# Kernel tuning notes

Hardware: AMD Instinct MI355X
Metric: run time of the kernel (lower is better)

The kernel has to match this reference:

```python
import jax, jax.numpy as jnp
import numpy as np

N_NODES = 50000
N_EDGES = 500000
N_GRAPHS = 64
IN_DIM = 64
HID = 128
N_LAYERS = 2
BN_EPS = 1e-5


def setup_inputs() -> dict:
    key = jax.random.key(0)
    ks = jax.random.split(key, 12)
    x = jax.random.normal(ks[0], (N_NODES, IN_DIM), dtype=jnp.float32)
    edge_index = jax.random.randint(ks[1], (2, N_EDGES), 0, N_NODES, dtype=jnp.int64)
    batch = jnp.sort(jax.random.randint(ks[2], (N_NODES,), 0, N_GRAPHS, dtype=jnp.int64))
    s = 0.05
    W_enc = jax.random.normal(ks[3], (IN_DIM, HID), dtype=jnp.float32) * s
    b_enc = jnp.zeros((HID,), dtype=jnp.float32)
    Wc = jax.random.normal(ks[4], (N_LAYERS, HID, HID), dtype=jnp.float32) * s
    bc = jnp.zeros((N_LAYERS, HID), dtype=jnp.float32)
    gamma = jnp.ones((N_LAYERS, HID), dtype=jnp.float32)
    beta = jnp.zeros((N_LAYERS, HID), dtype=jnp.float32)
    MID = HID // 2
    W1 = jax.random.normal(ks[5], (HID, MID), dtype=jnp.float32) * s
    b1 = jnp.zeros((MID,), dtype=jnp.float32)
    W2 = jax.random.normal(ks[6], (MID, 1), dtype=jnp.float32) * s
    b2 = jnp.zeros((1,), dtype=jnp.float32)
    return {"x": x, "edge_index": edge_index, "batch": batch,
            "W_enc": W_enc, "b_enc": b_enc, "Wc": Wc, "bc": bc,
            "gamma": gamma, "beta": beta, "W1": W1, "b1": b1,
            "W2": W2, "b2": b2}


def _gcn_conv(h, src, dst, norm, W, b, n_nodes):
    # h: [N, HID]; src/dst: [E+N] (self-loops included); norm: [E+N]
    h = h @ W                                   # [N, HID]
    msg = h[src] * norm[:, None]                # gather + normalize
    out = jax.ops.segment_sum(msg, dst, num_segments=n_nodes)  # scatter-add
    return out + b


def _batch_norm(h, g, b):
    mu = jnp.mean(h, axis=0)
    var = jnp.var(h, axis=0)
    return (h - mu) * jax.lax.rsqrt(var + BN_EPS) * g + b


def reference(x, edge_index, batch, W_enc, b_enc, Wc, bc, gamma, beta, W1, b1, W2, b2):
    n = x.shape[0]
    loop = jnp.arange(n, dtype=edge_index.dtype)
    src = jnp.concatenate([edge_index[0], loop])   # [E+N]
    dst = jnp.concatenate([edge_index[1], loop])
    # symmetric GCN normalization with self-loops: deg over target index
    deg = jax.ops.segment_sum(jnp.ones_like(dst, dtype=x.dtype), dst, num_segments=n)
    dinv = jax.lax.rsqrt(deg)                      # deg >= 1 due to self-loops
    norm = dinv[src] * dinv[dst]                   # [E+N]

    h = x @ W_enc + b_enc                          # node encoder
    for l in range(Wc.shape[0]):
        h = _gcn_conv(h, src, dst, norm, Wc[l], bc[l], n)
        h = _batch_norm(h, gamma[l], beta[l])
        h = jax.nn.relu(h)                         # dropout inactive (eval)

    # global mean pool over graphs
    pooled = jax.ops.segment_sum(h, batch, num_segments=N_GRAPHS)
    counts = jax.ops.segment_sum(jnp.ones((n,), dtype=h.dtype), batch, num_segments=N_GRAPHS)
    pooled = pooled / jnp.maximum(counts, 1.0)[:, None]

    z = jax.nn.relu(pooled @ W1 + b1)
    out = jax.nn.sigmoid(z @ W2 + b2)              # [B, 1]
    return out.squeeze(-1)                          # [B]
```

## Files before the change

kernel.cpp:

```cpp
#include <hip/hip_runtime.h>
#include <hip/hip_bf16.h>
#include <hip/hip_fp16.h>
#include <math.h>


typedef _Float16 f16x8 __attribute__((ext_vector_type(8)));
typedef float f32x4 __attribute__((ext_vector_type(4)));

__device__ inline unsigned pack2(float a, float b) {
  union { __half2 h; unsigned u; } p;
  p.h = __floats2half2_rn(a, b);
  return p.u;
}
__device__ inline float2 unpack2(unsigned u) {
  union { unsigned u; __half2 h; } p;
  p.u = u;
  return __half22float2(p.h);
}

__global__ __launch_bounds__(256) void k_init(int* __restrict__ deg,
                                              float* __restrict__ pooled,
                                              float* __restrict__ bnstat,
                                              int N) {
  int i = blockIdx.x * 256 + threadIdx.x;
  if (i < N) deg[i] = 1;
  if (i < 64 * 128) pooled[i] = 0.f;
  if (i < 4096) bnstat[i] = 0.f;
}

__global__ __launch_bounds__(256) void k_deg(const int* __restrict__ ei, int E,
                                             int* __restrict__ deg) {
  int i = blockIdx.x * 256 + threadIdx.x;
  if (i < E) atomicAdd(&deg[ei[E + i]], 1);
}

__global__ __launch_bounds__(256) void k_scan_a(const int* __restrict__ deg, int N,
                                                int* __restrict__ rowptr,
                                                int* __restrict__ blksum) {
  __shared__ int s[256];
  int t = threadIdx.x;
  int i = blockIdx.x * 256 + t;
  int v = (i < N) ? deg[i] : 0;
  s[t] = v;
  __syncthreads();
  for (int off = 1; off < 256; off <<= 1) {
    int x = (t >= off) ? s[t - off] : 0;
    __syncthreads();
    s[t] += x;
    __syncthreads();
  }
  if (i < N) rowptr[i] = s[t] - v;
  if (t == 255) blksum[blockIdx.x] = s[255];
}

__global__ __launch_bounds__(256) void k_scan_b(int* __restrict__ blksum, int nb) {
  __shared__ int s[256];
  int t = threadIdx.x;
  int v = (t < nb) ? blksum[t] : 0;
  s[t] = v;
  __syncthreads();
  for (int off = 1; off < 256; off <<= 1) {
    int x = (t >= off) ? s[t - off] : 0;
    __syncthreads();
    s[t] += x;
    __syncthreads();
  }
  if (t < nb) blksum[t] = s[t] - v;
}

__global__ __launch_bounds__(256) void k_scan_c(const int* __restrict__ deg, int N,
                                                int total,
                                                const int* __restrict__ blksum,
                                                int* __restrict__ rowptr,
                                                int* __restrict__ cursor,
                                                float* __restrict__ dinv) {
  int i = blockIdx.x * 256 + threadIdx.x;
  if (i < N) {
    int rp = rowptr[i] + blksum[blockIdx.x];
    rowptr[i] = rp;
    cursor[i] = rp;
    dinv[i] = rsqrtf((float)deg[i]);
  } else if (i == N) {
    rowptr[N] = total;
  }
}

__global__ __launch_bounds__(256) void k_fill(const int* __restrict__ ei, int E, int N,
                                              int* __restrict__ cursor,
                                              int* __restrict__ colx) {
  int i = blockIdx.x * 256 + threadIdx.x;
  if (i < E) {
    int s = ei[i];
    int d = ei[E + i];
    int pos = atomicAdd(&cursor[d], 1);
    colx[pos] = s;
  } else if (i < E + N) {
    int j = i - E;
    int pos = atomicAdd(&cursor[j], 1);
    colx[pos] = j;
  }
}

__global__ __launch_bounds__(128) void k_fold(const float* __restrict__ W_enc,
                                              const float* __restrict__ b_enc,
                                              const float* __restrict__ Wc0,
                                              unsigned short* __restrict__ MT,
                                              float* __restrict__ bfold) {
  int n = threadIdx.x;
  int k = blockIdx.x;
  const float* arow = (k < 64) ? (W_enc + (size_t)k * 128) : b_enc;
  float acc = 0.f;
  for (int j = 0; j < 128; j++) acc = fmaf(arow[j], Wc0[(size_t)j * 128 + n], acc);
  if (k < 64) ((__half*)MT)[(size_t)n * 64 + k] = __float2half(acc);
  else bfold[n] = acc;
}

__global__ __launch_bounds__(256) void k_wprep(const float* __restrict__ Wsrc,
                                               unsigned short* __restrict__ WT) {
  int i = blockIdx.x * 256 + threadIdx.x;
  int n = i & 127, k = i >> 7;
  ((__half*)WT)[(size_t)n * 128 + k] = __float2half(Wsrc[i]);
}

__global__ __launch_bounds__(256) void k_prep0(const float* __restrict__ x,
                                               const float* __restrict__ dinv,
                                               unsigned* __restrict__ xs2,
                                               int total ) {
  int i = blockIdx.x * 256 + threadIdx.x;
  if (i < total) {
    int row = i >> 4;
    float4 v = ((const float4*)x)[i];
    float d = dinv[row];
    uint2 o;
    o.x = pack2(v.x * d, v.y * d);
    o.y = pack2(v.z * d, v.w * d);
    ((uint2*)xs2)[i] = o;
  }
}

__global__ __launch_bounds__(256) void k_prep1(const unsigned short* __restrict__ H16,
                                               const float* __restrict__ scsh,
                                               const float* __restrict__ dinv,
                                               unsigned* __restrict__ hs2,
                                               int total ) {
  int i = blockIdx.x * 256 + threadIdx.x;
  if (i < total) {
    int row = i >> 5;
    int c4 = i & 31;
    uint2 hv = ((const uint2*)H16)[i];
    float2 h01 = unpack2(hv.x), h23 = unpack2(hv.y);
    float4 sc = ((const float4*)scsh)[c4];
    float4 sh = ((const float4*)(scsh + 128))[c4];
    float d = dinv[row];
    float a = fmaxf(fmaf(h01.x, sc.x, sh.x), 0.f) * d;
    float b = fmaxf(fmaf(h01.y, sc.y, sh.y), 0.f) * d;
    float c = fmaxf(fmaf(h23.x, sc.z, sh.z), 0.f) * d;
    float e = fmaxf(fmaf(h23.y, sc.w, sh.w), 0.f) * d;
    uint2 o;
    o.x = pack2(a, b);
    o.y = pack2(c, e);
    ((uint2*)hs2)[i] = o;
  }
}

__global__ __launch_bounds__(256) void k_agg0(const unsigned* __restrict__ xs,
                                              const int* __restrict__ rowptr,
                                              const int* __restrict__ colx,
                                              const float* __restrict__ dinv,
                                              unsigned* __restrict__ axh,
                                              float* __restrict__ w, int N) {
  int lane = threadIdx.x & 63;
  int wv = threadIdx.x >> 6;
  int half = lane >> 5;
  int l32 = lane & 31;
  int wid = blockIdx.x * 4 + wv;
  int nw = gridDim.x * 4;

  for (int base = 2 * wid; base < N; base += 2 * nw) {
    int i = base + half;
    if (i < N) {
      int beg = rowptr[i];
      int end = rowptr[i + 1];
      float sx = 0.f, sy = 0.f, sd = 0.f;
      int e = beg;
#pragma unroll 1
      for (; e + 4 <= end; e += 4) {
        int i0 = colx[e + 0], i1 = colx[e + 1], i2 = colx[e + 2], i3 = colx[e + 3];
        unsigned v0 = xs[(size_t)i0 * 32 + l32];
        unsigned v1 = xs[(size_t)i1 * 32 + l32];
        unsigned v2 = xs[(size_t)i2 * 32 + l32];
        unsigned v3 = xs[(size_t)i3 * 32 + l32];
        float d0 = dinv[i0], d1 = dinv[i1], d2 = dinv[i2], d3 = dinv[i3];
        float2 f0 = unpack2(v0), f1 = unpack2(v1), f2 = unpack2(v2), f3 = unpack2(v3);
        sx += (f0.x + f1.x) + (f2.x + f3.x);
        sy += (f0.y + f1.y) + (f2.y + f3.y);
        sd += (d0 + d1) + (d2 + d3);
      }
#pragma unroll 1
      for (; e < end; e++) {
        int sr = colx[e];
        float2 f = unpack2(xs[(size_t)sr * 32 + l32]);
        sx += f.x;
        sy += f.y;
        sd += dinv[sr];
      }
      float di = dinv[i];
      axh[(size_t)i * 32 + l32] = pack2(sx * di, sy * di);
      if (l32 == 0) w[i] = di * sd;
    }
  }
}

__global__ __launch_bounds__(256) void k_agg1(const uint2* __restrict__ hs,
                                              const int* __restrict__ rowptr,
                                              const int* __restrict__ colx,
                                              const float* __restrict__ dinv,
                                              uint2* __restrict__ a1h, int N) {
  int lane = threadIdx.x & 63;
  int wv = threadIdx.x >> 6;
  int half = lane >> 5;
  int l32 = lane & 31;
  int wid = blockIdx.x * 4 + wv;
  int nw = gridDim.x * 4;

  for (int base = 2 * wid; base < N; base += 2 * nw) {
    int i = base + half;
    if (i < N) {
      int beg = rowptr[i];
      int end = rowptr[i + 1];
      float4 s = make_float4(0.f, 0.f, 0.f, 0.f);
      int e = beg;
#pragma unroll 1
      for (; e + 4 <= end; e += 4) {
        int i0 = colx[e + 0], i1 = colx[e + 1], i2 = colx[e + 2], i3 = colx[e + 3];
        uint2 v0 = hs[(size_t)i0 * 32 + l32];
        uint2 v1 = hs[(size_t)i1 * 32 + l32];
        uint2 v2 = hs[(size_t)i2 * 32 + l32];
        uint2 v3 = hs[(size_t)i3 * 32 + l32];
        float2 a0 = unpack2(v0.x), b0 = unpack2(v0.y);
        float2 a1f = unpack2(v1.x), b1f = unpack2(v1.y);
        float2 a2 = unpack2(v2.x), b2 = unpack2(v2.y);
        float2 a3 = unpack2(v3.x), b3 = unpack2(v3.y);
        s.x += (a0.x + a1f.x) + (a2.x + a3.x);
        s.y += (a0.y + a1f.y) + (a2.y + a3.y);
        s.z += (b0.x + b1f.x) + (b2.x + b3.x);
        s.w += (b0.y + b1f.y) + (b2.y + b3.y);
      }
#pragma unroll 1
      for (; e < end; e++) {
        int sr = colx[e];
        uint2 v = hs[(size_t)sr * 32 + l32];
        float2 a = unpack2(v.x), b = unpack2(v.y);
        s.x += a.x; s.y += a.y; s.z += b.x; s.w += b.y;
      }
      float di = dinv[i];
      a1h[(size_t)i * 32 + l32] =
          make_uint2(pack2(s.x * di, s.y * di), pack2(s.z * di, s.w * di));
    }
  }
}

template <int K>
__global__ __launch_bounds__(256, 2) void k_gemm_f16(
    const unsigned short* __restrict__ Xh,
    const unsigned short* __restrict__ WT,
    const float* __restrict__ bias,
    const float* __restrict__ wvec,
    const float* __restrict__ bias2,
    float* __restrict__ stat,
    unsigned short* __restrict__ Yh,
    int N) {
  constexpr int KP = K + 8;
  constexpr int K8 = K / 8;
  __shared__ unsigned short Wl[128 * KP];
  __shared__ float red[4][2][128];

  for (int i = threadIdx.x; i < 128 * K8; i += 256) {
    int r = i / K8, c = i - r * K8;
    *(uint4*)&Wl[r * KP + c * 8] = ((const uint4*)(WT + (size_t)r * K))[c];
  }
  __syncthreads();

  int lane = threadIdx.x & 63;
  int wv = threadIdx.x >> 6;
  int l15 = lane & 15;
  int kg = lane >> 4;
  int tileRow = blockIdx.x * 64 + wv * 16;

  int arow = tileRow + l15;
  if (arow >= N) arow = N - 1;
  const unsigned short* xp = Xh + (size_t)arow * K + kg * 8;
  f16x8 af[K / 32];
#pragma unroll
  for (int j = 0; j < K / 32; j++) af[j] = *(const f16x8*)(xp + j * 32);

  f32x4 acc[8];
#pragma unroll
  for (int t = 0; t < 8; t++) acc[t] = {0.f, 0.f, 0.f, 0.f};

  const unsigned short* wb = &Wl[l15 * KP + kg * 8];
#pragma unroll
  for (int j = 0; j < K / 32; j++) {
#pragma unroll
    for (int t = 0; t < 8; t++) {
      f16x8 bf = *(const f16x8*)(wb + t * 16 * KP + j * 32);
      acc[t] = __builtin_amdgcn_mfma_f32_16x16x32_f16(af[j], bf, acc[t], 0, 0, 0);
    }
  }

  int rbase = tileRow + kg * 4;
  float wrow[4];
#pragma unroll
  for (int r = 0; r < 4; r++)
    wrow[r] = (wvec && rbase + r < N) ? wvec[rbase + r] : 0.f;

#pragma unroll
  for (int t = 0; t < 8; t++) {
    int ch = t * 16 + l15;
    float bb = bias[ch];
    float b2v = bias2 ? bias2[ch] : 0.f;
    float s = 0.f, q = 0.f;
#pragma unroll
    for (int r = 0; r < 4; r++) {
      int row = rbase + r;
      if (row < N) {
        float o = acc[t][r] + bb;
        if (wvec) o = fmaf(wrow[r], b2v, o);
        __half oh = __float2half(o);
        Yh[(size_t)row * 128 + ch] = *(unsigned short*)&oh;
        s += o;
        q += o * o;
      }
    }
    s += __shfl_xor(s, 16); s += __shfl_xor(s, 32);
    q += __shfl_xor(q, 16); q += __shfl_xor(q, 32);
    if (kg == 0) { red[wv][0][ch] = s; red[wv][1][ch] = q; }
  }
  __syncthreads();
  int st = threadIdx.x >> 7, ch2 = threadIdx.x & 127;
  float v = red[0][st][ch2] + red[1][st][ch2] + red[2][st][ch2] + red[3][st][ch2];
  atomicAdd(&stat[(blockIdx.x & 7) * 256 + st * 128 + ch2], v);
}

__global__ __launch_bounds__(128) void k_bnfinal(const float* __restrict__ stat,
                                                 const float* __restrict__ gamma,
                                                 const float* __restrict__ beta,
                                                 float invN,
                                                 float* __restrict__ scsh) {
  int c = threadIdx.x;
  float ssum = 0.f, qsum = 0.f;
#pragma unroll
  for (int rep = 0; rep < 8; rep++) {
    ssum += stat[rep * 256 + c];
    qsum += stat[rep * 256 + 128 + c];
  }
  float mu = ssum * invN;
  float var = qsum * invN - mu * mu;
  float sc = rsqrtf(var + 1e-5f) * gamma[c];
  scsh[c] = sc;
  scsh[128 + c] = beta[c] - mu * sc;
}

__global__ __launch_bounds__(128) void k_gstart(const int* __restrict__ batch, int N,
                                                int* __restrict__ gstart) {
  int g = threadIdx.x;
  if (g <= 64) {
    int lo = 0, hi = N;
    while (lo < hi) {
      int mid = (lo + hi) >> 1;
      if (batch[mid] < g) lo = mid + 1;
      else hi = mid;
    }
    gstart[g] = lo;
  }
}

__global__ __launch_bounds__(128) void k_pool(const unsigned short* __restrict__ H16,
                                              const float* __restrict__ scsh,
                                              const int* __restrict__ gstart,
                                              float* __restrict__ pooled) {
  int g = blockIdx.x >> 3;
  int part = blockIdx.x & 7;
  int c = threadIdx.x;
  float sc = scsh[c], sh = scsh[128 + c];
  int beg = gstart[g], end = gstart[g + 1];
  int len = end - beg;
  int pbeg = beg + (len * part) / 8;
  int pend = beg + (len * (part + 1)) / 8;
  float s = 0.f;
  for (int r = pbeg; r < pend; r++) {
    float v = __half2float(((const __half*)H16)[(size_t)r * 128 + c]);
    s += fmaxf(fmaf(v, sc, sh), 0.f);
  }
  atomicAdd(&pooled[g * 128 + c], s);
}

__global__ __launch_bounds__(256) void k_mlp(const float* __restrict__ pooled,
                                             const int* __restrict__ gstart,
                                             const float* __restrict__ W1,
                                             const float* __restrict__ b1,
                                             const float* __restrict__ W2,
                                             const float* __restrict__ b2,
                                             float* __restrict__ out) {
  __shared__ float P[64 * 128];
  __shared__ float Z[64 * 64];
  for (int i = threadIdx.x; i < 64 * 128; i += 256) {
    int g = i >> 7;
    int cnt = gstart[g + 1] - gstart[g];
    P[i] = pooled[i] / (float)(cnt > 1 ? cnt : 1);
  }
  __syncthreads();
  for (int i = threadIdx.x; i < 64 * 64; i += 256) {
    int g = i >> 6, m = i & 63;
    float acc = b1[m];
    for (int k = 0; k < 128; k++) acc += P[(g << 7) + k] * W1[k * 64 + m];
    Z[i] = fmaxf(acc, 0.f);
  }
  __syncthreads();
  if (threadIdx.x < 64) {
    int g = threadIdx.x;
    float acc = b2[0];
    for (int m = 0; m < 64; m++) acc += Z[(g << 6) + m] * W2[m];
    out[g] = 1.f / (1.f + expf(-acc));
  }
}


extern "C" void kernel_launch(void* const* d_in, const int* in_sizes, int n_in,
                              void* d_out, int out_size, void* d_ws, size_t ws_size,
                              hipStream_t stream) {
  const float* x      = (const float*)d_in[0];
  const int*   ei     = (const int*)d_in[1];
  const int*   batch  = (const int*)d_in[2];
  const float* W_enc  = (const float*)d_in[3];
  const float* b_enc  = (const float*)d_in[4];
  const float* Wc     = (const float*)d_in[5];
  const float* bc     = (const float*)d_in[6];
  const float* gamma  = (const float*)d_in[7];
  const float* beta   = (const float*)d_in[8];
  const float* W1     = (const float*)d_in[9];
  const float* b1     = (const float*)d_in[10];
  const float* W2     = (const float*)d_in[11];
  const float* b2     = (const float*)d_in[12];
  float* out = (float*)d_out;

  const int N = in_sizes[2];
  const int E = in_sizes[1] / 2;
  const int NL = in_sizes[6] / 128;

  size_t off = 0;
  auto alloc = [&](size_t bytes) {
    void* p = (char*)d_ws + off;
    off += (bytes + 255) & ~(size_t)255;
    return p;
  };
  unsigned short* h16 = (unsigned short*)alloc((size_t)N * 128 * 2);
  int*   deg    = (int*)alloc((size_t)N * 4);
  float* dinv   = (float*)alloc((size_t)N * 4);
  int*   rowptr = (int*)alloc((size_t)(N + 1) * 4);
  int*   cursor = (int*)alloc((size_t)N * 4);
  int*   colx   = (int*)alloc((size_t)(E + N) * 4);
  int*   blksum = (int*)alloc(1024 * 4);
  float* bnstat = (float*)alloc(4096 * 4);
  float* scsh   = (float*)alloc(512 * 4);
  float* pooled = (float*)alloc(64 * 128 * 4);
  int*   gstart = (int*)alloc(65 * 4);
  unsigned short* MT  = (unsigned short*)alloc(128 * 64 * 2);
  unsigned short* WT1 = (unsigned short*)alloc(128 * 128 * 2);
  float* bfold  = (float*)alloc(128 * 4);
  unsigned* xs  = (unsigned*)alloc((size_t)N * 64 * 2);
  unsigned* hs  = (unsigned*)alloc((size_t)N * 128 * 2);
  unsigned* axh = (unsigned*)alloc((size_t)N * 64 * 2);
  uint2*    a1h = (uint2*)alloc((size_t)N * 128 * 2);
  float* wv     = (float*)alloc((size_t)N * 4);

  int nbN = (N + 255) / 256;

  k_init<<<nbN, 256, 0, stream>>>(deg, pooled, bnstat, N);
  k_deg<<<(E + 255) / 256, 256, 0, stream>>>(ei, E, deg);
  k_scan_a<<<nbN, 256, 0, stream>>>(deg, N, rowptr, blksum);
  k_scan_b<<<1, 256, 0, stream>>>(blksum, nbN);
  k_scan_c<<<(N + 1 + 255) / 256, 256, 0, stream>>>(deg, N, E + N, blksum,
                                                    rowptr, cursor, dinv);
  k_fill<<<(E + N + 255) / 256, 256, 0, stream>>>(ei, E, N, cursor, colx);
  k_fold<<<65, 128, 0, stream>>>(W_enc, b_enc, Wc, MT, bfold);

  int tiles = (N + 63) / 64;

  k_prep0<<<(N * 16 + 255) / 256, 256, 0, stream>>>(x, dinv, xs, N * 16);
  k_agg0<<<2048, 256, 0, stream>>>(xs, rowptr, colx, dinv, axh, wv, N);
  k_gemm_f16<64><<<tiles, 256, 0, stream>>>(
      (const unsigned short*)axh, MT, bc, wv, bfold, bnstat, h16, N);
  k_bnfinal<<<1, 128, 0, stream>>>(bnstat, gamma, beta, 1.f / (float)N, scsh);

  for (int l = 1; l < NL; l++) {
    k_wprep<<<64, 256, 0, stream>>>(Wc + (size_t)l * 128 * 128, WT1);
    k_prep1<<<(N * 32 + 255) / 256, 256, 0, stream>>>(
        h16, scsh + (l - 1) * 256, dinv, hs, N * 32);
    k_agg1<<<2048, 256, 0, stream>>>((const uint2*)hs, rowptr, colx, dinv,
                                     a1h, N);
    k_gemm_f16<128><<<tiles, 256, 0, stream>>>(
        (const unsigned short*)a1h, WT1, bc + l * 128, nullptr, nullptr,
        bnstat + l * 2048, h16, N);
    k_bnfinal<<<1, 128, 0, stream>>>(bnstat + l * 2048, gamma + l * 128,
                                     beta + l * 128, 1.f / (float)N,
                                     scsh + l * 256);
  }

  k_gstart<<<1, 128, 0, stream>>>(batch, N, gstart);
  k_pool<<<64 * 8, 128, 0, stream>>>(h16, scsh + (NL - 1) * 256, gstart, pooled);
  k_mlp<<<1, 256, 0, stream>>>(pooled, gstart, W1, b1, W2, b2, out);
}
```

Before: 295.1 us.

## Merge setup kernels, fold BN finalize into consumers, widen agg0 gathers

Combines init, weight folding, layer-1 weight prep and graph-start search into one setup launch, and merges CSR fill with input prescaling. Removes the separate BN finalize and gstart kernels by recomputing scale/shift inside prep1 and pool blocks. Changes agg0 to 16 lanes per node with 8-byte loads, handling four nodes per wave. Fewer launches reduce per-kernel overhead, but every block now redundantly recomputes the BN statistics.

```diff
diff --git a/kernel.cpp b/kernel.cpp
--- a/kernel.cpp
+++ b/kernel.cpp
@@ -18,14 +18,55 @@
   return __half22float2(p.h);
 }
 
-__global__ __launch_bounds__(256) void k_init(int* __restrict__ deg,
-                                              float* __restrict__ pooled,
-                                              float* __restrict__ bnstat,
-                                              int N) {
-  int i = blockIdx.x * 256 + threadIdx.x;
-  if (i < N) deg[i] = 1;
-  if (i < 64 * 128) pooled[i] = 0.f;
-  if (i < 4096) bnstat[i] = 0.f;
+__global__ __launch_bounds__(256) void k_setup(
+    int* __restrict__ deg, float* __restrict__ pooled,
+    float* __restrict__ bnstat, int statTotal, int N, int nbN,
+    const float* __restrict__ W_enc, const float* __restrict__ b_enc,
+    const float* __restrict__ Wc, unsigned short* __restrict__ MT,
+    float* __restrict__ bfold, int NL,
+    const float* __restrict__ Wc1, unsigned short* __restrict__ WT1,
+    const int* __restrict__ batch, int* __restrict__ gstart) {
+  int b = blockIdx.x;
+  if (b < nbN) {
+    int i = b * 256 + threadIdx.x;
+    if (i < N) deg[i] = 1;
+    if (i < 64 * 128) pooled[i] = 0.f;
+    if (i < statTotal) bnstat[i] = 0.f;
+    return;
+  }
+  b -= nbN;
+  if (b < 65) {
+    if (threadIdx.x < 128) {
+      int n = threadIdx.x;
+      int k = b;
+      const float* arow = (k < 64) ? (W_enc + (size_t)k * 128) : b_enc;
+      float acc = 0.f;
+      for (int j = 0; j < 128; j++)
+        acc = fmaf(arow[j], Wc[(size_t)j * 128 + n], acc);
+      if (k < 64) ((__half*)MT)[(size_t)n * 64 + k] = __float2half(acc);
+      else bfold[n] = acc;
+    }
+    return;
+  }
+  b -= 65;
+  if (b < 64) {
+    if (NL > 1) {
+      int i = b * 256 + threadIdx.x;
+      int n = i & 127, k = i >> 7;
+      ((__half*)WT1)[(size_t)n * 128 + k] = __float2half(Wc1[i]);
+    }
+    return;
+  }
+  int g = threadIdx.x;
+  if (g <= 64) {
+    int lo = 0, hi = N;
+    while (lo < hi) {
+      int mid = (lo + hi) >> 1;
+      if (batch[mid] < g) lo = mid + 1;
+      else hi = mid;
+    }
+    gstart[g] = lo;
+  }
 }
 
 __global__ __launch_bounds__(256) void k_deg(const int* __restrict__ ei, int E,
@@ -85,49 +126,29 @@
   }
 }
 
-__global__ __launch_bounds__(256) void k_fill(const int* __restrict__ ei, int E, int N,
-                                              int* __restrict__ cursor,
-                                              int* __restrict__ colx) {
-  int i = blockIdx.x * 256 + threadIdx.x;
-  if (i < E) {
-    int s = ei[i];
-    int d = ei[E + i];
-    int pos = atomicAdd(&cursor[d], 1);
-    colx[pos] = s;
-  } else if (i < E + N) {
-    int j = i - E;
-    int pos = atomicAdd(&cursor[j], 1);
-    colx[pos] = j;
-  }
-}
-
-__global__ __launch_bounds__(128) void k_fold(const float* __restrict__ W_enc,
-                                              const float* __restrict__ b_enc,
-                                              const float* __restrict__ Wc0,
-                                              unsigned short* __restrict__ MT,
-                                              float* __restrict__ bfold) {
-  int n = threadIdx.x;
-  int k = blockIdx.x;
-  const float* arow = (k < 64) ? (W_enc + (size_t)k * 128) : b_enc;
-  float acc = 0.f;
-  for (int j = 0; j < 128; j++) acc = fmaf(arow[j], Wc0[(size_t)j * 128 + n], acc);
-  if (k < 64) ((__half*)MT)[(size_t)n * 64 + k] = __float2half(acc);
-  else bfold[n] = acc;
-}
-
-__global__ __launch_bounds__(256) void k_wprep(const float* __restrict__ Wsrc,
-                                               unsigned short* __restrict__ WT) {
-  int i = blockIdx.x * 256 + threadIdx.x;
-  int n = i & 127, k = i >> 7;
-  ((__half*)WT)[(size_t)n * 128 + k] = __float2half(Wsrc[i]);
-}
-
-__global__ __launch_bounds__(256) void k_prep0(const float* __restrict__ x,
-                                               const float* __restrict__ dinv,
-                                               unsigned* __restrict__ xs2,
-                                               int total ) {
-  int i = blockIdx.x * 256 + threadIdx.x;
-  if (i < total) {
+__global__ __launch_bounds__(256) void k_fillprep(
+    const int* __restrict__ ei, int E, int N, int nbEN,
+    int* __restrict__ cursor, int* __restrict__ colx,
+    const float* __restrict__ x, const float* __restrict__ dinv,
+    unsigned* __restrict__ xs2) {
+  int b = blockIdx.x;
+  if (b < nbEN) {
+    int i = b * 256 + threadIdx.x;
+    if (i < E) {
+      int s = ei[i];
+      int d = ei[E + i];
+      int pos = atomicAdd(&cursor[d], 1);
+      colx[pos] = s;
+    } else if (i < E + N) {
+      int j = i - E;
+      int pos = atomicAdd(&cursor[j], 1);
+      colx[pos] = j;
+    }
+    return;
+  }
+  b -= nbEN;
+  int i = b * 256 + threadIdx.x;
+  if (i < N * 16) {
     int row = i >> 4;
     float4 v = ((const float4*)x)[i];
     float d = dinv[row];
@@ -139,18 +160,37 @@
 }
 
 __global__ __launch_bounds__(256) void k_prep1(const unsigned short* __restrict__ H16,
-                                               const float* __restrict__ scsh,
+                                               const float* __restrict__ stat,
+                                               const float* __restrict__ gamma,
+                                               const float* __restrict__ beta,
+                                               float invN,
                                                const float* __restrict__ dinv,
                                                unsigned* __restrict__ hs2,
                                                int total ) {
+  __shared__ float scsh[256];
+  if (threadIdx.x < 128) {
+    int c = threadIdx.x;
+    float ss = 0.f, qs = 0.f;
+#pragma unroll
+    for (int r = 0; r < 8; r++) {
+      ss += stat[r * 256 + c];
+      qs += stat[r * 256 + 128 + c];
+    }
+    float mu = ss * invN;
+    float var = qs * invN - mu * mu;
+    float sc = rsqrtf(var + 1e-5f) * gamma[c];
+    scsh[c] = sc;
+    scsh[128 + c] = beta[c] - mu * sc;
+  }
+  __syncthreads();
   int i = blockIdx.x * 256 + threadIdx.x;
   if (i < total) {
     int row = i >> 5;
     int c4 = i & 31;
     uint2 hv = ((const uint2*)H16)[i];
     float2 h01 = unpack2(hv.x), h23 = unpack2(hv.y);
-    float4 sc = ((const float4*)scsh)[c4];
-    float4 sh = ((const float4*)(scsh + 128))[c4];
+    float4 sc = *(const float4*)&scsh[c4 * 4];
+    float4 sh = *(const float4*)&scsh[128 + c4 * 4];
     float d = dinv[row];
     float a = fmaxf(fmaf(h01.x, sc.x, sh.x), 0.f) * d;
     float b = fmaxf(fmaf(h01.y, sc.y, sh.y), 0.f) * d;
@@ -163,50 +203,56 @@
   }
 }
 
-__global__ __launch_bounds__(256) void k_agg0(const unsigned* __restrict__ xs,
+__global__ __launch_bounds__(256) void k_agg0(const uint2* __restrict__ xs,
                                               const int* __restrict__ rowptr,
                                               const int* __restrict__ colx,
                                               const float* __restrict__ dinv,
-                                              unsigned* __restrict__ axh,
+                                              uint2* __restrict__ axh,
                                               float* __restrict__ w, int N) {
   int lane = threadIdx.x & 63;
   int wv = threadIdx.x >> 6;
-  int half = lane >> 5;
-  int l32 = lane & 31;
+  int grp = lane >> 4;
+  int l16 = lane & 15;
   int wid = blockIdx.x * 4 + wv;
   int nw = gridDim.x * 4;
 
-  for (int base = 2 * wid; base < N; base += 2 * nw) {
-    int i = base + half;
+  for (int base = 4 * wid; base < N; base += 4 * nw) {
+    int i = base + grp;
     if (i < N) {
       int beg = rowptr[i];
       int end = rowptr[i + 1];
-      float sx = 0.f, sy = 0.f, sd = 0.f;
+      float s0 = 0.f, s1 = 0.f, s2 = 0.f, s3 = 0.f, sd = 0.f;
       int e = beg;
 #pragma unroll 1
       for (; e + 4 <= end; e += 4) {
         int i0 = colx[e + 0], i1 = colx[e + 1], i2 = colx[e + 2], i3 = colx[e + 3];
-        unsigned v0 = xs[(size_t)i0 * 32 + l32];
-        unsigned v1 = xs[(size_t)i1 * 32 + l32];
-        unsigned v2 = xs[(size_t)i2 * 32 + l32];
-        unsigned v3 = xs[(size_t)i3 * 32 + l32];
+        uint2 v0 = xs[(size_t)i0 * 16 + l16];
+        uint2 v1 = xs[(size_t)i1 * 16 + l16];
+        uint2 v2 = xs[(size_t)i2 * 16 + l16];
+        uint2 v3 = xs[(size_t)i3 * 16 + l16];
         float d0 = dinv[i0], d1 = dinv[i1], d2 = dinv[i2], d3 = dinv[i3];
-        float2 f0 = unpack2(v0), f1 = unpack2(v1), f2 = unpack2(v2), f3 = unpack2(v3);
-        sx += (f0.x + f1.x) + (f2.x + f3.x);
-        sy += (f0.y + f1.y) + (f2.y + f3.y);
+        float2 a0 = unpack2(v0.x), b0 = unpack2(v0.y);
+        float2 a1 = unpack2(v1.x), b1 = unpack2(v1.y);
+        float2 a2 = unpack2(v2.x), b2 = unpack2(v2.y);
+        float2 a3 = unpack2(v3.x), b3 = unpack2(v3.y);
+        s0 += (a0.x + a1.x) + (a2.x + a3.x);
+        s1 += (a0.y + a1.y) + (a2.y + a3.y);
+        s2 += (b0.x + b1.x) + (b2.x + b3.x);
+        s3 += (b0.y + b1.y) + (b2.y + b3.y);
         sd += (d0 + d1) + (d2 + d3);
       }
 #pragma unroll 1
       for (; e < end; e++) {
         int sr = colx[e];
-        float2 f = unpack2(xs[(size_t)sr * 32 + l32]);
-        sx += f.x;
-        sy += f.y;
+        uint2 v = xs[(size_t)sr * 16 + l16];
+        float2 a = unpack2(v.x), b = unpack2(v.y);
+        s0 += a.x; s1 += a.y; s2 += b.x; s3 += b.y;
         sd += dinv[sr];
       }
       float di = dinv[i];
-      axh[(size_t)i * 32 + l32] = pack2(sx * di, sy * di);
-      if (l32 == 0) w[i] = di * sd;
+      axh[(size_t)i * 16 + l16] =
+          make_uint2(pack2(s0 * di, s1 * di), pack2(s2 * di, s3 * di));
+      if (l16 == 0) w[i] = di * sd;
     }
   }
 }
@@ -260,6 +306,13 @@
   }
 }
 
+__global__ __launch_bounds__(256) void k_wprep(const float* __restrict__ Wsrc,
+                                               unsigned short* __restrict__ WT) {
+  int i = blockIdx.x * 256 + threadIdx.x;
+  int n = i & 127, k = i >> 7;
+  ((__half*)WT)[(size_t)n * 128 + k] = __float2half(Wsrc[i]);
+}
+
 template <int K>
 __global__ __launch_bounds__(256, 2) void k_gemm_f16(
     const unsigned short* __restrict__ Xh,
@@ -342,47 +395,27 @@
   atomicAdd(&stat[(blockIdx.x & 7) * 256 + st * 128 + ch2], v);
 }
 
-__global__ __launch_bounds__(128) void k_bnfinal(const float* __restrict__ stat,
-                                                 const float* __restrict__ gamma,
-                                                 const float* __restrict__ beta,
-                                                 float invN,
-                                                 float* __restrict__ scsh) {
-  int c = threadIdx.x;
-  float ssum = 0.f, qsum = 0.f;
-#pragma unroll
-  for (int rep = 0; rep < 8; rep++) {
-    ssum += stat[rep * 256 + c];
-    qsum += stat[rep * 256 + 128 + c];
-  }
-  float mu = ssum * invN;
-  float var = qsum * invN - mu * mu;
-  float sc = rsqrtf(var + 1e-5f) * gamma[c];
-  scsh[c] = sc;
-  scsh[128 + c] = beta[c] - mu * sc;
-}
-
-__global__ __launch_bounds__(128) void k_gstart(const int* __restrict__ batch, int N,
-                                                int* __restrict__ gstart) {
-  int g = threadIdx.x;
-  if (g <= 64) {
-    int lo = 0, hi = N;
-    while (lo < hi) {
-      int mid = (lo + hi) >> 1;
-      if (batch[mid] < g) lo = mid + 1;
-      else hi = mid;
-    }
-    gstart[g] = lo;
-  }
-}
-
 __global__ __launch_bounds__(128) void k_pool(const unsigned short* __restrict__ H16,
-                                              const float* __restrict__ scsh,
+                                              const float* __restrict__ stat,
+                                              const float* __restrict__ gamma,
+                                              const float* __restrict__ beta,
+                                              float invN,
                                               const int* __restrict__ gstart,
                                               float* __restrict__ pooled) {
+  int c = threadIdx.x;
+  float ss = 0.f, qs = 0.f;
+#pragma unroll
+  for (int r = 0; r < 8; r++) {
+    ss += stat[r * 256 + c];
+    qs += stat[r * 256 + 128 + c];
+  }
+  float mu = ss * invN;
+  float var = qs * invN - mu * mu;
+  float sc = rsqrtf(var + 1e-5f) * gamma[c];
+  float sh = beta[c] - mu * sc;
+
   int g = blockIdx.x >> 3;
   int part = blockIdx.x & 7;
-  int c = threadIdx.x;
-  float sc = scsh[c], sh = scsh[128 + c];
   int beg = gstart[g], end = gstart[g + 1];
   int len = end - beg;
   int pbeg = beg + (len * part) / 8;
@@ -461,8 +494,7 @@
   int*   cursor = (int*)alloc((size_t)N * 4);
   int*   colx   = (int*)alloc((size_t)(E + N) * 4);
   int*   blksum = (int*)alloc(1024 * 4);
-  float* bnstat = (float*)alloc(4096 * 4);
-  float* scsh   = (float*)alloc(512 * 4);
+  float* bnstat = (float*)alloc((size_t)NL * 2048 * 4);
   float* pooled = (float*)alloc(64 * 128 * 4);
   int*   gstart = (int*)alloc(65 * 4);
   unsigned short* MT  = (unsigned short*)alloc(128 * 64 * 2);
@@ -475,39 +507,43 @@
   float* wv     = (float*)alloc((size_t)N * 4);
 
   int nbN = (N + 255) / 256;
-
-  k_init<<<nbN, 256, 0, stream>>>(deg, pooled, bnstat, N);
+  int nbEN = (E + N + 255) / 256;
+  float invN = 1.f / (float)N;
+
+  k_setup<<<nbN + 130, 256, 0, stream>>>(
+      deg, pooled, bnstat, NL * 2048, N, nbN, W_enc, b_enc, Wc, MT, bfold, NL,
+      Wc + (size_t)128 * 128, WT1, batch, gstart);
   k_deg<<<(E + 255) / 256, 256, 0, stream>>>(ei, E, deg);
   k_scan_a<<<nbN, 256, 0, stream>>>(deg, N, rowptr, blksum);
   k_scan_b<<<1, 256, 0, stream>>>(blksum, nbN);
   k_scan_c<<<(N + 1 + 255) / 256, 256, 0, stream>>>(deg, N, E + N, blksum,
                                                     rowptr, cursor, dinv);
-  k_fill<<<(E + N + 255) / 256, 256, 0, stream>>>(ei, E, N, cursor, colx);
-  k_fold<<<65, 128, 0, stream>>>(W_enc, b_enc, Wc, MT, bfold);
+  k_fillprep<<<nbEN + (N * 16 + 255) / 256, 256, 0, stream>>>(
+      ei, E, N, nbEN, cursor, colx, x, dinv, xs);
 
   int tiles = (N + 63) / 64;
 
-  k_prep0<<<(N * 16 + 255) / 256, 256, 0, stream>>>(x, dinv, xs, N * 16);
-  k_agg0<<<2048, 256, 0, stream>>>(xs, rowptr, colx, dinv, axh, wv, N);
+  k_agg0<<<2048, 256, 0, stream>>>((const uint2*)xs, rowptr, colx, dinv,
+                                   (uint2*)axh, wv, N);
   k_gemm_f16<64><<<tiles, 256, 0, stream>>>(
       (const unsigned short*)axh, MT, bc, wv, bfold, bnstat, h16, N);
-  k_bnfinal<<<1, 128, 0, stream>>>(bnstat, gamma, beta, 1.f / (float)N, scsh);
 
   for (int l = 1; l < NL; l++) {
-    k_wprep<<<64, 256, 0, stream>>>(Wc + (size_t)l * 128 * 128, WT1);
+    if (l > 1)
+      k_wprep<<<64, 256, 0, stream>>>(Wc + (size_t)l * 128 * 128, WT1);
     k_prep1<<<(N * 32 + 255) / 256, 256, 0, stream>>>(
-        h16, scsh + (l - 1) * 256, dinv, hs, N * 32);
+        h16, bnstat + (l - 1) * 2048, gamma + (l - 1) * 128,
+        beta + (l - 1) * 128, invN, dinv, hs, N * 32);
     k_agg1<<<2048, 256, 0, stream>>>((const uint2*)hs, rowptr, colx, dinv,
                                      a1h, N);
     k_gemm_f16<128><<<tiles, 256, 0, stream>>>(
         (const unsigned short*)a1h, WT1, bc + l * 128, nullptr, nullptr,
         bnstat + l * 2048, h16, N);
-    k_bnfinal<<<1, 128, 0, stream>>>(bnstat + l * 2048, gamma + l * 128,
-                                     beta + l * 128, 1.f / (float)N,
-                                     scsh + l * 256);
-  }
-
-  k_gstart<<<1, 128, 0, stream>>>(batch, N, gstart);
-  k_pool<<<64 * 8, 128, 0, stream>>>(h16, scsh + (NL - 1) * 256, gstart, pooled);
+  }
+
+  k_pool<<<64 * 8, 128, 0, stream>>>(h16, bnstat + (NL - 1) * 2048,
+                                     gamma + (NL - 1) * 128,
+                                     beta + (NL - 1) * 128, invN, gstart,
+                                     pooled);
   k_mlp<<<1, 256, 0, stream>>>(pooled, gstart, W1, b1, W2, b2, out);
 }
```

Result: faster. 278.0 us (-5.8%).
